# Optimization experiments

Measured on AMD Instinct MI355X. Metric: run time of the kernel, lower is better.

## Reference

```python
import jax, jax.numpy as jnp
import numpy as np

B, S, D_IN, D_OUT = 4, 2048, 1024, 1024


def setup_inputs() -> dict:
    key = jax.random.key(0)
    ks = jax.random.split(key, 7)
    return {
        "X": jax.random.normal(ks[0], (B, S, D_IN), dtype=jnp.float32),
        "Wq": jax.random.normal(ks[1], (D_IN, D_OUT), dtype=jnp.float32) * (1.0 / np.sqrt(D_IN)),
        "bq": jax.random.normal(ks[2], (D_OUT,), dtype=jnp.float32) * 0.02,
        "Wk": jax.random.normal(ks[3], (D_IN, D_OUT), dtype=jnp.float32) * (1.0 / np.sqrt(D_IN)),
        "bk": jax.random.normal(ks[4], (D_OUT,), dtype=jnp.float32) * 0.02,
        "Wv": jax.random.normal(ks[5], (D_IN, D_OUT), dtype=jnp.float32) * (1.0 / np.sqrt(D_IN)),
        "bv": jax.random.normal(ks[6], (D_OUT,), dtype=jnp.float32) * 0.02,
    }


def reference(X, Wq, bq, Wk, bk, Wv, bv):
    # Linear projections (torch Linear: x @ W^T + b; here W stored as [in,out])
    Q = X @ Wq + bq  # [B,S,D]
    K = X @ Wk + bk
    V = X @ Wv + bv
    dk = jnp.sqrt(jnp.asarray(D_OUT, dtype=X.dtype))
    # Raw scores, lower-triangular ZEROING (not -inf), scale, softmax over keys.
    S_ = jnp.einsum('bqd,bkd->bqk', Q, K)
    S_ = jnp.tril(S_) / dk
    A = jax.nn.softmax(S_, axis=2)  # [B,S,S]
    # Faithful to torch.einsum('ijk,ijl->ijl', A, V): reduces A over k, scales V.
    out = jnp.einsum('bqk,bql->bql', A, V)
    return out
```

## Files before the change

### kernel.cpp

```cpp
#include <hip/hip_runtime.h>
#include <hip/hip_bf16.h>

#define DIN  1024
#define DOUT 1024
#define MROWS 8192

#define BM 128
#define BN 128
#define BK 64
#define NKT (DIN / BK)

typedef __attribute__((ext_vector_type(8))) short short8;
typedef __attribute__((ext_vector_type(4))) float f32x4;

__device__ __forceinline__ ushort f2bf(float f) {
    union { float f; unsigned u; } x; x.f = f;
    unsigned u = x.u + 0x7fffu + ((x.u >> 16) & 1u);
    return (ushort)(u >> 16);
}

__global__ void prep_kernel(const float* __restrict__ X, ushort* __restrict__ Xb,
                            const float* __restrict__ W, ushort* __restrict__ Wt) {
    __shared__ float tile[32][33];
    const int b = blockIdx.x;
    if (b < 2048) {
        const float4* X4 = (const float4*)X;
        ushort4* O4 = (ushort4*)Xb;
        const int n4 = MROWS * DIN / 4;
        for (int idx = b * 256 + threadIdx.x; idx < n4; idx += 2048 * 256) {
            float4 v = X4[idx];
            ushort4 o;
            o.x = f2bf(v.x); o.y = f2bf(v.y); o.z = f2bf(v.z); o.w = f2bf(v.w);
            O4[idx] = o;
        }
    } else {
        const int t = b - 2048;
        const int bx = (t & 31) * 32;
        const int by = (t >> 5) * 32;
        const int tx = threadIdx.x & 31;
        const int ty = threadIdx.x >> 5;
#pragma unroll
        for (int i = 0; i < 32; i += 8)
            tile[ty + i][tx] = W[(size_t)(by + ty + i) * DOUT + (bx + tx)];
        __syncthreads();
#pragma unroll
        for (int i = 0; i < 32; i += 8)
            Wt[(size_t)(bx + ty + i) * DIN + (by + tx)] = f2bf(tile[tx][ty + i]);
    }
}

__global__ __launch_bounds__(256, 2) void gemm_bias(
    const ushort* __restrict__ Xb,
    const ushort* __restrict__ Wt,
    const float* __restrict__ bias,
    float* __restrict__ out)
{
    __shared__ ushort As[2][BM * BK];
    __shared__ ushort Bs[2][BN * BK];

    const int tid  = threadIdx.x;
    const int lane = tid & 63;
    const int wid  = tid >> 6;
    const int wr   = wid >> 1;
    const int wc   = wid & 1;

    const int bid = blockIdx.x;
    const int swz = (bid & 7) * 64 + (bid >> 3);
    const int bm = (swz >> 3) * BM;
    const int bn = (swz & 7) * BN;

    auto stage = [&](int b, int kt) {
#pragma unroll
        for (int i = 0; i < 4; ++i) {
            const int c   = i * 256 + tid;
            const int rl  = c >> 3;
            const int scc = (c & 7) ^ (rl & 7);
            __builtin_amdgcn_global_load_lds(
                (const __attribute__((address_space(1))) void*)(Xb + (size_t)(bm + rl) * DIN + kt * BK + scc * 8),
                (__attribute__((address_space(3))) void*)(&As[b][(i * 256 + wid * 64) * 8]),
                16, 0, 0);
        }
#pragma unroll
        for (int i = 0; i < 4; ++i) {
            const int c   = i * 256 + tid;
            const int rl  = c >> 3;
            const int scc = (c & 7) ^ (rl & 7);
            __builtin_amdgcn_global_load_lds(
                (const __attribute__((address_space(1))) void*)(Wt + (size_t)(bn + rl) * DIN + kt * BK + scc * 8),
                (__attribute__((address_space(3))) void*)(&Bs[b][(i * 256 + wid * 64) * 8]),
                16, 0, 0);
        }
    };

    f32x4 acc[4][4];
#pragma unroll
    for (int i = 0; i < 4; ++i)
#pragma unroll
        for (int j = 0; j < 4; ++j)
            acc[i][j] = (f32x4){0.f, 0.f, 0.f, 0.f};

    const int am  = wr * 64 + (lane & 15);
    const int bnr = wc * 64 + (lane & 15);

    stage(0, 0);
    __syncthreads();

    for (int t = 0; t < NKT; ++t) {
        const int buf = t & 1;
        if (t < NKT - 1) stage(buf ^ 1, t + 1);
#pragma unroll
        for (int ks = 0; ks < 2; ++ks) {
            short8 af[4], bfr[4];
            const int sc = ((ks * 4 + (lane >> 4)) ^ (lane & 7)) * 8;
#pragma unroll
            for (int i = 0; i < 4; ++i)
                af[i] = *(const short8*)(&As[buf][(am + i * 16) * BK + sc]);
#pragma unroll
            for (int j = 0; j < 4; ++j)
                bfr[j] = *(const short8*)(&Bs[buf][(bnr + j * 16) * BK + sc]);
#pragma unroll
            for (int i = 0; i < 4; ++i)
#pragma unroll
                for (int j = 0; j < 4; ++j)
                    acc[i][j] = __builtin_amdgcn_mfma_f32_16x16x32_bf16(af[i], bfr[j], acc[i][j], 0, 0, 0);
        }
        __syncthreads();
    }

    const int crow = bm + wr * 64 + (lane >> 4) * 4;
    const int ccol = bn + wc * 64 + (lane & 15);
#pragma unroll
    for (int j = 0; j < 4; ++j) {
        const int col = ccol + j * 16;
        const float bval = bias[col];
#pragma unroll
        for (int i = 0; i < 4; ++i) {
#pragma unroll
            for (int r = 0; r < 4; ++r)
                out[(size_t)(crow + i * 16 + r) * DOUT + col] = acc[i][j][r] + bval;
        }
    }
}

__global__ void gemm_naive(const float* __restrict__ X, const float* __restrict__ W,
                           const float* __restrict__ b, float* __restrict__ out) {
    int n = blockIdx.x * blockDim.x + threadIdx.x;
    int m = blockIdx.y;
    float acc = b[n];
    for (int k = 0; k < DIN; ++k)
        acc += X[(size_t)m * DIN + k] * W[(size_t)k * DOUT + n];
    out[(size_t)m * DOUT + n] = acc;
}

extern "C" void kernel_launch(void* const* d_in, const int* in_sizes, int n_in,
                              void* d_out, int out_size, void* d_ws, size_t ws_size,
                              hipStream_t stream) {
    const float* X  = (const float*)d_in[0];
    const float* Wv = (const float*)d_in[5];
    const float* bv = (const float*)d_in[6];
    float* out = (float*)d_out;

    const size_t xb_elems = (size_t)MROWS * DIN;
    const size_t wt_elems = (size_t)DOUT * DIN;
    const size_t needed = (xb_elems + wt_elems) * sizeof(ushort);

    if (ws_size < needed) {
        dim3 g(DOUT / 256, MROWS);
        gemm_naive<<<g, 256, 0, stream>>>(X, Wv, bv, out);
        return;
    }

    ushort* Xb = (ushort*)d_ws;
    ushort* Wt = Xb + xb_elems;

    prep_kernel<<<2048 + 1024, 256, 0, stream>>>(X, Xb, Wv, Wt);
    gemm_bias<<<512, 256, 0, stream>>>(Xb, Wt, bv, out);
}
```

Before: 41.23 us.

## Load B fragments directly from global into registers, bypassing LDS

Removes the shared-memory staging buffer for the transposed weight tile. Each wave now loads its B fragments straight from global memory into registers, 16 short8 per lane per pair of k-tiles. Only A is still staged in LDS with double buffering. This halves LDS traffic and footprint, but B reads are no longer shared between the two waves of a row, so global/L2 traffic goes up, register pressure rises, and the B loads sit un-overlapped right before the MFMAs.

```diff
diff --git a/kernel.cpp b/kernel.cpp
--- a/kernel.cpp
+++ b/kernel.cpp
@@ -56,20 +56,20 @@
     float* __restrict__ out)
 {
     __shared__ ushort As[2][BM * BK];
-    __shared__ ushort Bs[2][BN * BK];
 
     const int tid  = threadIdx.x;
     const int lane = tid & 63;
     const int wid  = tid >> 6;
     const int wr   = wid >> 1;
     const int wc   = wid & 1;
+    const int g    = lane >> 4;
 
     const int bid = blockIdx.x;
     const int swz = (bid & 7) * 64 + (bid >> 3);
     const int bm = (swz >> 3) * BM;
     const int bn = (swz & 7) * BN;
 
-    auto stage = [&](int b, int kt) {
+    auto stageA = [&](int b, int kt) {
 #pragma unroll
         for (int i = 0; i < 4; ++i) {
             const int c   = i * 256 + tid;
@@ -78,16 +78,6 @@
             __builtin_amdgcn_global_load_lds(
                 (const __attribute__((address_space(1))) void*)(Xb + (size_t)(bm + rl) * DIN + kt * BK + scc * 8),
                 (__attribute__((address_space(3))) void*)(&As[b][(i * 256 + wid * 64) * 8]),
-                16, 0, 0);
-        }
-#pragma unroll
-        for (int i = 0; i < 4; ++i) {
-            const int c   = i * 256 + tid;
-            const int rl  = c >> 3;
-            const int scc = (c & 7) ^ (rl & 7);
-            __builtin_amdgcn_global_load_lds(
-                (const __attribute__((address_space(1))) void*)(Wt + (size_t)(bn + rl) * DIN + kt * BK + scc * 8),
-                (__attribute__((address_space(3))) void*)(&Bs[b][(i * 256 + wid * 64) * 8]),
                 16, 0, 0);
         }
     };
@@ -99,32 +89,41 @@
         for (int j = 0; j < 4; ++j)
             acc[i][j] = (f32x4){0.f, 0.f, 0.f, 0.f};
 
-    const int am  = wr * 64 + (lane & 15);
-    const int bnr = wc * 64 + (lane & 15);
+    const int am = wr * 64 + (lane & 15);
+    const ushort* bSrc = Wt + (size_t)(bn + wc * 64 + (lane & 15)) * DIN + g * 8;
 
-    stage(0, 0);
+    stageA(0, 0);
     __syncthreads();
 
-    for (int t = 0; t < NKT; ++t) {
-        const int buf = t & 1;
-        if (t < NKT - 1) stage(buf ^ 1, t + 1);
+    short8 bf[4][4];
+
+#pragma unroll 1
+    for (int p = 0; p < 8; ++p) {
 #pragma unroll
-        for (int ks = 0; ks < 2; ++ks) {
-            short8 af[4], bfr[4];
-            const int sc = ((ks * 4 + (lane >> 4)) ^ (lane & 7)) * 8;
-#pragma unroll
-            for (int i = 0; i < 4; ++i)
-                af[i] = *(const short8*)(&As[buf][(am + i * 16) * BK + sc]);
+        for (int kh = 0; kh < 4; ++kh)
 #pragma unroll
             for (int j = 0; j < 4; ++j)
-                bfr[j] = *(const short8*)(&Bs[buf][(bnr + j * 16) * BK + sc]);
+                bf[kh][j] = *(const short8*)(bSrc + (size_t)j * 16 * DIN + p * 128 + kh * 32);
 #pragma unroll
-            for (int i = 0; i < 4; ++i)
+        for (int tt = 0; tt < 2; ++tt) {
+            const int t   = 2 * p + tt;
+            const int buf = t & 1;
+            if (t < NKT - 1) stageA(buf ^ 1, t + 1);
 #pragma unroll
-                for (int j = 0; j < 4; ++j)
-                    acc[i][j] = __builtin_amdgcn_mfma_f32_16x16x32_bf16(af[i], bfr[j], acc[i][j], 0, 0, 0);
+            for (int ks = 0; ks < 2; ++ks) {
+                short8 af[4];
+                const int sc = ((ks * 4 + g) ^ (lane & 7)) * 8;
+#pragma unroll
+                for (int i = 0; i < 4; ++i)
+                    af[i] = *(const short8*)(&As[buf][(am + i * 16) * BK + sc]);
+#pragma unroll
+                for (int i = 0; i < 4; ++i)
+#pragma unroll
+                    for (int j = 0; j < 4; ++j)
+                        acc[i][j] = __builtin_amdgcn_mfma_f32_16x16x32_bf16(af[i], bf[tt * 2 + ks][j], acc[i][j], 0, 0, 0);
+            }
+            __syncthreads();
         }
-        __syncthreads();
     }
 
     const int crow = bm + wr * 64 + (lane >> 4) * 4;
```

Measured after the change: 54.69 us. 1.33x slower.
